# Optimization experiments

Measured on AMD Instinct MI355X. Metric: run time of the kernel, lower is better.

Reference implementation:

```python
import jax, jax.numpy as jnp
import numpy as np
from jax import lax

B, N, CH, CIN, H, W = 4, 256, 128, 1024, 120, 160
SRC = 256      # source rows of the (B, CH, 256, 1) relation feature map
MIN_BOX = 5    # boxes smaller than this (at half res) are skipped


def _conv(x, w, b):
    # 3x3 SAME conv, NCHW / OIHW, matching torch Conv2d(pad=1)
    return lax.conv_general_dilated(x, w, (1, 1), 'SAME',
                                    dimension_numbers=('NCHW', 'OIHW', 'NCHW')) + b[None, :, None, None]


def _boxes(k, xmax, ymax):
    k1, k2, k3, k4 = jax.random.split(k, 4)
    x1 = jax.random.randint(k1, (B, N), 0, xmax - 40)
    y1 = jax.random.randint(k2, (B, N), 0, ymax - 40)
    x2 = jnp.clip(x1 + jax.random.randint(k3, (B, N), 10, 80), 0, xmax)
    y2 = jnp.clip(y1 + jax.random.randint(k4, (B, N), 10, 80), 0, ymax)
    return jnp.stack([x1, y1, x2, y2], -1)


def setup_inputs() -> dict:
    key = jax.random.key(0)
    ks = jax.random.split(key, 24)
    s = 0.05
    rn = lambda k, shp: (s * jax.random.normal(k, shp)).astype(jnp.float32)
    return {
        'range_attention_maps': jax.random.normal(ks[0], (B, CH, H, W), jnp.float32),
        'tuple_features': jax.random.normal(ks[1], (B, CIN, N), jnp.float32),
        # rel_embedding: two 1x1 convs stored as matrices
        'rel_w1': rn(ks[2], (CH, CIN)), 'rel_b1': rn(ks[3], (CH,)),
        'rel_w2': rn(ks[4], (CH, CH)),  'rel_b2': rn(ks[5], (CH,)),
        'dmc_w': rn(ks[6], (4, 2 * CH, CH, 3, 3)), 'dmc_b': rn(ks[7], (4, 2 * CH)),
        # TriGraph image collectors: [0,1] Conv2d(2ch->ch), [2,3] Conv2d(ch->ch)
        'imc_w01': rn(ks[8], (2, CH, 2 * CH, 3, 3)), 'imc_b01': rn(ks[9], (2, CH)),
        'imc_w23': rn(ks[10], (2, CH, CH, 3, 3)),    'imc_b23': rn(ks[11], (2, CH)),
        # TriGraph relation collectors: same layout as image collectors
        'rmc_w01': rn(ks[12], (2, CH, 2 * CH, 3, 3)), 'rmc_b01': rn(ks[13], (2, CH)),
        'rmc_w23': rn(ks[14], (2, CH, CH, 3, 3)),     'rmc_b23': rn(ks[15], (2, CH)),
        # final embedding: Conv2d(2ch->ch,3) -> ReLU -> Conv2d(ch->ch,3)
        'emb_w1': rn(ks[16], (CH, 2 * CH, 3, 3)), 'emb_b1': rn(ks[17], (CH,)),
        'emb_w2': rn(ks[18], (CH, CH, 3, 3)),     'emb_b2': rn(ks[19], (CH,)),
        # bbox: [sx1,sy1,sx2,sy2, ox1,oy1,ox2,oy2] at full res (coords < 2W x 2H)
        'bbox': jnp.concatenate([_boxes(ks[20], 2 * W, 2 * H),
                                 _boxes(ks[21], 2 * W, 2 * H)], -1).astype(jnp.int32),
    }


def _interp_scatter(rel_map, bbox):
    # rel_map: (B, CH, SRC) -- the (SRC,1) relation feature map per image.
    # torch F.interpolate(mode='nearest') of a (SRC,1) map to (h,w): column 0 is
    # replicated across width; output row k reads source row floor(k*SRC/h).
    sub = bbox[..., :4] // 2
    obj = bbox[..., 4:] // 2
    sh, sw = sub[..., 3] - sub[..., 1], sub[..., 2] - sub[..., 0]
    oh, ow = obj[..., 3] - obj[..., 1], obj[..., 2] - obj[..., 0]
    # the torch loop `continue`s unless BOTH sub and obj boxes are big enough
    valid = (sh >= MIN_BOX) & (sw >= MIN_BOX) & (oh >= MIN_BOX) & (ow >= MIN_BOX)

    ys = jnp.arange(H)
    xs = jnp.arange(W)
    bi = jnp.arange(B)[:, None, None]

    def contrib(box, h):
        x1, y1, x2, y2 = box[..., 0], box[..., 1], box[..., 2], box[..., 3]
        ym = (ys >= y1[..., None]) & (ys < y2[..., None]) & valid[..., None]   # (B,N,H)
        xm = ((xs >= x1[..., None]) & (xs < x2[..., None])).astype(rel_map.dtype)  # (B,N,W)
        idx = jnp.clip((ys - y1[..., None]) * SRC // jnp.maximum(h, 1)[..., None], 0, SRC - 1)
        rows = rel_map[bi, :, idx] * ym[..., None].astype(rel_map.dtype)       # (B,N,H,CH)
        # scatter-add every box's resized patch into the full map
        return jnp.einsum('bjyc,bjx->bcyx', rows, xm)

    return contrib(sub, sh) + contrib(obj, oh)  # (B, CH, H, W)


def reference(range_attention_maps, tuple_features,
              rel_w1, rel_b1, rel_w2, rel_b2,
              dmc_w, dmc_b, imc_w01, imc_b01, imc_w23, imc_b23,
              rmc_w01, rmc_b01, rmc_w23, rmc_b23,
              emb_w1, emb_b1, emb_w2, emb_b2, bbox):
    relu = jax.nn.relu
    # rel_embedding on (B, CIN, N, 1): 1x1 convs == channel matmuls
    hmid = relu(jnp.einsum('oc,bcn->bon', rel_w1, tuple_features) + rel_b1[None, :, None])
    rel_map = jnp.einsum('oc,bcn->bon', rel_w2, hmid) + rel_b2[None, :, None]  # (B,CH,SRC)

    rel = _interp_scatter(rel_map, bbox)          # (B,CH,H,W)
    img = range_attention_maps                    # (B,CH,H,W)
    dep = jnp.concatenate([img, rel], axis=1)     # (B,2CH,H,W)

    # TriGraph, max_iters = 2; all messages computed from pre-update state
    for i in range(2):
        dm = (_conv(img, dmc_w[i], dmc_b[i]) + _conv(rel, dmc_w[2 + i], dmc_b[2 + i])) * 0.5
        im = (_conv(dep, imc_w01[i], imc_b01[i]) + _conv(rel, imc_w23[i], imc_b23[i])) * 0.5
        rm = (_conv(dep, rmc_w01[i], rmc_b01[i]) + _conv(img, rmc_w23[i], rmc_b23[i])) * 0.5
        dep = relu(dep + dm)
        img = relu(img + im)
        rel = relu(rel + rm)

    out = _conv(relu(_conv(dep, emb_w1, emb_b1)), emb_w2, emb_b2)  # (B,CH,H,W)
    return out
```

## Files before the change

kernel.cpp:

```cpp
#include <hip/hip_runtime.h>

#define BB 4
#define NTUP 256
#define CHN 128
#define CINN 1024
#define HH 120
#define WW 160
#define HWSZ (HH*WW)
#define SRCN 256
#define CT 512

typedef __attribute__((ext_vector_type(8))) _Float16 f16x8;
typedef __attribute__((ext_vector_type(4))) float f32x4;

__device__ __forceinline__ unsigned short f2h(float f) {
  _Float16 h = (_Float16)f;
  return __builtin_bit_cast(unsigned short, h);
}
__device__ __forceinline__ float h2f(unsigned short u) {
  _Float16 h = __builtin_bit_cast(_Float16, u);
  return (float)h;
}

__global__ __launch_bounds__(256) void k_hmid(const float* __restrict__ tf,
    const float* __restrict__ w1, const float* __restrict__ b1,
    float* __restrict__ hmid) {
  int bc = blockIdx.x;
  int b = bc >> 7, c = bc & 127;
  int n = threadIdx.x;
  const float* wrow = w1 + (size_t)c * CINN;
  const float* xcol = tf + (size_t)b * CINN * NTUP + n;
  float acc = 0.f;
#pragma unroll 4
  for (int k = 0; k < CINN; ++k)
    acc += wrow[k] * xcol[(size_t)k * NTUP];
  acc += b1[c];
  hmid[(size_t)bc * NTUP + n] = fmaxf(acc, 0.f);
}

__global__ __launch_bounds__(256) void k_w2t(const float* __restrict__ w2,
                                             float* __restrict__ w2t) {
  int i = blockIdx.x * 256 + threadIdx.x;
  if (i >= CHN * CHN) return;
  int o = i >> 7, c = i & 127;
  w2t[c * CHN + o] = w2[i];
}

__global__ __launch_bounds__(128) void k_relmap(const float* __restrict__ hmid,
    const float* __restrict__ w2t, const float* __restrict__ b2,
    float* __restrict__ rmT) {
  int n = blockIdx.x, b = blockIdx.y, o = threadIdx.x;
  const float* hc = hmid + (size_t)b * CHN * NTUP + n;
  float acc = 0.f;
#pragma unroll 4
  for (int c = 0; c < CHN; ++c)
    acc += hc[(size_t)c * NTUP] * w2t[c * CHN + o];
  rmT[((size_t)b * SRCN + n) * CHN + o] = acc + b2[o];
}

__global__ __launch_bounds__(256) void k_img_init(const float* __restrict__ img,
                                                  unsigned short* __restrict__ S) {
  int xt = blockIdx.x;
  int y  = blockIdx.y;
  int b  = blockIdx.z;
  __shared__ float t[128 * 33];
  int x0 = xt * 32;
  for (int i = threadIdx.x; i < 128 * 32; i += 256) {
    int c = i >> 5, x = i & 31;
    t[c * 33 + x] = img[(((size_t)b * CHN + c) * HH + y) * WW + x0 + x];
  }
  __syncthreads();
  for (int j = threadIdx.x; j < 32 * 128; j += 256) {
    int x = j >> 7, c = j & 127;
    unsigned short v = f2h(t[c * 33 + x]);
    size_t base = ((size_t)b * HWSZ + (size_t)y * WW + x0 + x) * CT;
    S[base + c] = v;
    S[base + 256 + c] = v;
  }
}

__global__ __launch_bounds__(256) void k_scatter(const float* __restrict__ rmT,
    const int* __restrict__ bbox, unsigned short* __restrict__ S) {
  int y  = blockIdx.x;
  int b  = blockIdx.y;
  int x0 = blockIdx.z * 80;
  __shared__ float row[80 * 129];
  int t = threadIdx.x;
  int c = t & 127, xo = t >> 7;
  for (int i = t; i < 80 * 128; i += 256) { int x = i >> 7, cc = i & 127; row[x * 129 + cc] = 0.f; }
  __syncthreads();
  const int* bb = bbox + (size_t)b * NTUP * 8;
  for (int j = 0; j < NTUP; ++j) {
    const int* bp = bb + j * 8;
    int sx1 = bp[0] >> 1, sy1 = bp[1] >> 1, sx2 = bp[2] >> 1, sy2 = bp[3] >> 1;
    int ox1 = bp[4] >> 1, oy1 = bp[5] >> 1, ox2 = bp[6] >> 1, oy2 = bp[7] >> 1;
    int sh = sy2 - sy1, sw = sx2 - sx1, oh = oy2 - oy1, ow = ox2 - ox1;
    if (!((sh >= 5) && (sw >= 5) && (oh >= 5) && (ow >= 5))) continue;
    if (y >= sy1 && y < sy2) {
      int a = max(sx1, x0), e = min(sx2, x0 + 80);
      if (a < e) {
        int idx = min((y - sy1) * SRCN / sh, SRCN - 1);
        float col = rmT[((size_t)b * SRCN + idx) * CHN + c];
        int start = a + ((xo - a) & 1);
        for (int x = start; x < e; x += 2) row[(x - x0) * 129 + c] += col;
      }
    }
    if (y >= oy1 && y < oy2) {
      int a = max(ox1, x0), e = min(ox2, x0 + 80);
      if (a < e) {
        int idx = min((y - oy1) * SRCN / oh, SRCN - 1);
        float col = rmT[((size_t)b * SRCN + idx) * CHN + c];
        int start = a + ((xo - a) & 1);
        for (int x = start; x < e; x += 2) row[(x - x0) * 129 + c] += col;
      }
    }
  }
  __syncthreads();
  for (int j2 = t; j2 < 80 * 128; j2 += 256) {
    int x = j2 >> 7, c2 = j2 & 127;
    unsigned short v = f2h(row[x * 129 + c2]);
    size_t base = ((size_t)b * HWSZ + (size_t)y * WW + x0 + x) * CT;
    S[base + 128 + c2] = v;
    S[base + 384 + c2] = v;
  }
}

__global__ void k_pack(const float* __restrict__ wA, int ICa,
                       const float* __restrict__ wB, int ICb,
                       int OC, unsigned short* __restrict__ dst) {
  int ICP = ICa + ICb;
  int total = 9 * OC * ICP;
  int i = blockIdx.x * 256 + threadIdx.x;
  if (i >= total) return;
  int tap = i / (OC * ICP); int r = i % (OC * ICP);
  int oc = r / ICP; int icp = r % ICP;
  int dy = tap / 3, dx = tap % 3;
  float v;
  if (icp < ICa) v = wA[((size_t)(oc * ICa + icp) * 3 + dy) * 3 + dx];
  else           v = wB[((size_t)(oc * ICb + (icp - ICa)) * 3 + dy) * 3 + dx];
  dst[i] = f2h(v);
}

struct ConvGroup {
  const unsigned short* w;
  const float* biasA;
  const float* biasB;
  const unsigned short* res;
  int ICP, OCg, oc_wbase;
  int c0a, na, c0b;
  int res_c0, out_c0;
  float scale;
  int relu;
};
struct ConvCommon {
  const unsigned short* in; int Ct_in;
  unsigned short* outb; int Ct_out;
  float* outf;
};
struct ConvParams { ConvCommon c; ConvGroup g[4]; };

__global__ __launch_bounds__(512) void k_conv(ConvParams P) {
  const ConvGroup G = P.g[blockIdx.z];
  const int b  = blockIdx.y;
  const int y0 = blockIdx.x * 2;
  const int t = threadIdx.x;
  const int wave = t >> 6, lane = t & 63;
  const int wm = wave & 1, wn = wave >> 1;
  const int r = wn >> 1;
  const int xbase = (wn & 1) * 80;
  const int ln = lane & 15, kg = lane >> 4;

  __shared__ unsigned short lds[4 * 162 * 32];

  f32x4 acc[4][5];
#pragma unroll
  for (int m = 0; m < 4; ++m)
#pragma unroll
    for (int n = 0; n < 5; ++n) acc[m][n] = (f32x4)(0.f);

  const int nch = G.ICP >> 5;
  for (int k = 0; k < nch; ++k) {
    const int icp0 = k << 5;
    const int cg = (icp0 < G.na) ? (G.c0a + icp0) : (G.c0b + icp0 - G.na);
    __syncthreads();
    if (t < 32) {
      int icg = t & 3, hx = (t >> 2) & 1, rw = t >> 3;
      uint4 z = {0u, 0u, 0u, 0u};
      *(uint4*)&lds[((rw * 162) + (hx ? 161 : 0)) * 32 + icg * 8] = z;
    }
#pragma unroll
    for (int s = 0; s < 5; ++s) {
      int id = t + (s << 9);
      int icg = id & 3;
      int xx = (id >> 2) % 160;
      int rw = (id >> 2) / 160;
      int ry = y0 - 1 + rw;
      uint4 v = {0u, 0u, 0u, 0u};
      if (ry >= 0 && ry < HH)
        v = *(const uint4*)(P.c.in + ((size_t)b * HWSZ + (size_t)ry * WW + xx) * P.c.Ct_in + cg + icg * 8);
      *(uint4*)&lds[((rw * 162) + xx + 1) * 32 + icg * 8] = v;
    }
    __syncthreads();
#pragma unroll
    for (int dy = 0; dy < 3; ++dy) {
      const int lrow = (r + dy) * 162;
#pragma unroll
      for (int dx = 0; dx < 3; ++dx) {
        const int tap = dy * 3 + dx;
        const unsigned short* wp = G.w +
            ((size_t)(tap * G.OCg + G.oc_wbase + wm * 64 + ln)) * G.ICP + icp0 + kg * 8;
        f16x8 A[4];
#pragma unroll
        for (int m = 0; m < 4; ++m)
          A[m] = *(const f16x8*)(wp + (size_t)m * 16 * G.ICP);
#pragma unroll
        for (int nf = 0; nf < 5; ++nf) {
          const f16x8 Bv = *(const f16x8*)(&lds[(lrow + xbase + nf * 16 + dx + ln) * 32 + kg * 8]);
#pragma unroll
          for (int m = 0; m < 4; ++m)
            acc[m][nf] = __builtin_amdgcn_mfma_f32_16x16x32_f16(A[m], Bv, acc[m][nf], 0, 0, 0);
        }
      }
    }
  }

  const int yy = y0 + r;
#pragma unroll
  for (int m = 0; m < 4; ++m) {
    const int ocl = wm * 64 + m * 16 + (kg << 2);
    const int ocw = G.oc_wbase + ocl;
    float bias[4];
#pragma unroll
    for (int q = 0; q < 4; ++q)
      bias[q] = G.biasA[ocw + q] + (G.biasB ? G.biasB[ocw + q] : 0.f);
#pragma unroll
    for (int nf = 0; nf < 5; ++nf) {
      const int x = xbase + nf * 16 + ln;
      const size_t pix = (size_t)b * HWSZ + (size_t)yy * WW + x;
      float v[4];
#pragma unroll
      for (int q = 0; q < 4; ++q)
        v[q] = (acc[m][nf][q] + bias[q]) * G.scale;
      if (G.res) {
        const unsigned short* rp = G.res + pix * P.c.Ct_in + G.res_c0 + ocw;
        uint2 rv = *(const uint2*)rp;
        v[0] += h2f((unsigned short)(rv.x & 0xffffu));
        v[1] += h2f((unsigned short)(rv.x >> 16));
        v[2] += h2f((unsigned short)(rv.y & 0xffffu));
        v[3] += h2f((unsigned short)(rv.y >> 16));
      }
      if (G.relu) {
#pragma unroll
        for (int q = 0; q < 4; ++q) v[q] = fmaxf(v[q], 0.f);
      }
      if (P.c.outf) {
#pragma unroll
        for (int q = 0; q < 4; ++q)
          P.c.outf[(((size_t)b * CHN + ocw + q) * HH + yy) * WW + x] = v[q];
      } else {
        uint2 pk;
        pk.x = (unsigned)f2h(v[0]) | ((unsigned)f2h(v[1]) << 16);
        pk.y = (unsigned)f2h(v[2]) | ((unsigned)f2h(v[3]) << 16);
        *(uint2*)(P.c.outb + pix * P.c.Ct_out + G.out_c0 + ocw) = pk;
      }
    }
  }
}

extern "C" void kernel_launch(void* const* d_in, const int* in_sizes, int n_in,
                              void* d_out, int out_size, void* d_ws, size_t ws_size,
                              hipStream_t stream) {
  const float* ram     = (const float*)d_in[0];
  const float* tf      = (const float*)d_in[1];
  const float* w1      = (const float*)d_in[2];
  const float* b1      = (const float*)d_in[3];
  const float* w2      = (const float*)d_in[4];
  const float* b2      = (const float*)d_in[5];
  const float* dmc_w   = (const float*)d_in[6];
  const float* dmc_b   = (const float*)d_in[7];
  const float* imc_w01 = (const float*)d_in[8];
  const float* imc_b01 = (const float*)d_in[9];
  const float* imc_w23 = (const float*)d_in[10];
  const float* imc_b23 = (const float*)d_in[11];
  const float* rmc_w01 = (const float*)d_in[12];
  const float* rmc_b01 = (const float*)d_in[13];
  const float* rmc_w23 = (const float*)d_in[14];
  const float* rmc_b23 = (const float*)d_in[15];
  const float* emb_w1  = (const float*)d_in[16];
  const float* emb_b1  = (const float*)d_in[17];
  const float* emb_w2  = (const float*)d_in[18];
  const float* emb_b2  = (const float*)d_in[19];
  const int*   bbox    = (const int*)d_in[20];
  float* out = (float*)d_out;

  char* ws = (char*)d_ws;
  size_t off = 0;
  auto alloc = [&](size_t bytes) -> void* {
    void* p = ws + off;
    off += (bytes + 255) & ~(size_t)255;
    return p;
  };
  unsigned short* SA = (unsigned short*)alloc((size_t)BB * HWSZ * CT * 2);
  unsigned short* SB = (unsigned short*)alloc((size_t)BB * HWSZ * CT * 2);
  unsigned short* T  = (unsigned short*)alloc((size_t)BB * HWSZ * 128 * 2);
  float* hmid = (float*)alloc((size_t)BB * CHN * NTUP * 4);
  float* rmT  = (float*)alloc((size_t)BB * SRCN * CHN * 4);
  float* w2t  = (float*)alloc((size_t)CHN * CHN * 4);
  unsigned short* pw_dm[2], *pw_im[2], *pw_rm[2];
  for (int i = 0; i < 2; ++i) pw_dm[i] = (unsigned short*)alloc((size_t)9 * 256 * 256 * 2);
  for (int i = 0; i < 2; ++i) pw_im[i] = (unsigned short*)alloc((size_t)9 * 128 * 384 * 2);
  for (int i = 0; i < 2; ++i) pw_rm[i] = (unsigned short*)alloc((size_t)9 * 128 * 384 * 2);
  unsigned short* pw_e1 = (unsigned short*)alloc((size_t)9 * 128 * 256 * 2);
  unsigned short* pw_e2 = (unsigned short*)alloc((size_t)9 * 128 * 128 * 2);
  if (off > ws_size) return;

  k_hmid<<<BB * CHN, 256, 0, stream>>>(tf, w1, b1, hmid);
  k_w2t<<<(CHN * CHN + 255) / 256, 256, 0, stream>>>(w2, w2t);
  k_relmap<<<dim3(NTUP, BB), 128, 0, stream>>>(hmid, w2t, b2, rmT);
  k_img_init<<<dim3(5, HH, BB), 256, 0, stream>>>(ram, SA);
  k_scatter<<<dim3(HH, BB, 2), 256, 0, stream>>>(rmT, bbox, SA);

  auto pk = [&](const float* wA, int ICa, const float* wB, int ICb, int OC,
                unsigned short* dst) {
    int total = 9 * OC * (ICa + ICb);
    k_pack<<<(total + 255) / 256, 256, 0, stream>>>(wA, ICa, wB, ICb, OC, dst);
  };
  for (int i = 0; i < 2; ++i) {
    pk(dmc_w + (size_t)i * 256 * 128 * 9, 128, dmc_w + (size_t)(2 + i) * 256 * 128 * 9, 128, 256, pw_dm[i]);
    pk(imc_w01 + (size_t)i * 128 * 256 * 9, 256, imc_w23 + (size_t)i * 128 * 128 * 9, 128, 128, pw_im[i]);
    pk(rmc_w01 + (size_t)i * 128 * 256 * 9, 256, rmc_w23 + (size_t)i * 128 * 128 * 9, 128, 128, pw_rm[i]);
  }
  pk(emb_w1, 256, nullptr, 0, 128, pw_e1);
  pk(emb_w2, 128, nullptr, 0, 128, pw_e2);

  for (int i = 0; i < 2; ++i) {
    const unsigned short* Sin = (i == 0) ? SA : SB;
    unsigned short* Sout      = (i == 0) ? SB : SA;
    ConvParams cp;
    cp.c.in = Sin; cp.c.Ct_in = CT; cp.c.outb = Sout; cp.c.Ct_out = CT; cp.c.outf = nullptr;
    for (int h = 0; h < 2; ++h) {
      ConvGroup& g = cp.g[h];
      g.w = pw_dm[i]; g.biasA = dmc_b + (size_t)i * 256; g.biasB = dmc_b + (size_t)(2 + i) * 256;
      g.res = Sin; g.ICP = 256; g.OCg = 256; g.oc_wbase = h * 128;
      g.c0a = 256; g.na = 128; g.c0b = 384;
      g.res_c0 = 0; g.out_c0 = 0; g.scale = 0.5f; g.relu = 1;
    }
    {
      ConvGroup& g = cp.g[2];
      g.w = pw_im[i]; g.biasA = imc_b01 + (size_t)i * 128; g.biasB = imc_b23 + (size_t)i * 128;
      g.res = Sin; g.ICP = 384; g.OCg = 128; g.oc_wbase = 0;
      g.c0a = 0; g.na = 256; g.c0b = 384;
      g.res_c0 = 256; g.out_c0 = 256; g.scale = 0.5f; g.relu = 1;
    }
    {
      ConvGroup& g = cp.g[3];
      g.w = pw_rm[i]; g.biasA = rmc_b01 + (size_t)i * 128; g.biasB = rmc_b23 + (size_t)i * 128;
      g.res = Sin; g.ICP = 384; g.OCg = 128; g.oc_wbase = 0;
      g.c0a = 0; g.na = 256; g.c0b = 256;
      g.res_c0 = 384; g.out_c0 = 384; g.scale = 0.5f; g.relu = 1;
    }
    k_conv<<<dim3(HH / 2, BB, 4), 512, 0, stream>>>(cp);
  }

  {
    ConvParams cp;
    cp.c.in = SA; cp.c.Ct_in = CT; cp.c.outb = T; cp.c.Ct_out = 128; cp.c.outf = nullptr;
    ConvGroup& g = cp.g[0];
    g.w = pw_e1; g.biasA = emb_b1; g.biasB = nullptr; g.res = nullptr;
    g.ICP = 256; g.OCg = 128; g.oc_wbase = 0;
    g.c0a = 0; g.na = 256; g.c0b = 0;
    g.res_c0 = -1; g.out_c0 = 0; g.scale = 1.f; g.relu = 1;
    k_conv<<<dim3(HH / 2, BB, 1), 512, 0, stream>>>(cp);
  }
  {
    ConvParams cp;
    cp.c.in = T; cp.c.Ct_in = 128; cp.c.outb = nullptr; cp.c.Ct_out = 0; cp.c.outf = out;
    ConvGroup& g = cp.g[0];
    g.w = pw_e2; g.biasA = emb_b2; g.biasB = nullptr; g.res = nullptr;
    g.ICP = 128; g.OCg = 128; g.oc_wbase = 0;
    g.c0a = 0; g.na = 128; g.c0b = 0;
    g.res_c0 = -1; g.out_c0 = 0; g.scale = 1.f; g.relu = 0;
    k_conv<<<dim3(HH / 2, BB, 1), 512, 0, stream>>>(cp);
  }
}
```

Baseline: 1.494 ms.

## Use channel-blocked activation layout and fragment-packed weights in conv kernel

```diff
diff --git a/kernel.cpp b/kernel.cpp
--- a/kernel.cpp
+++ b/kernel.cpp
@@ -8,7 +8,8 @@
 #define WW 160
 #define HWSZ (HH*WW)
 #define SRCN 256
-#define CT 512
+#define ROWH (WW*32)
+#define CBS  (HH*ROWH)
 
 typedef __attribute__((ext_vector_type(8))) _Float16 f16x8;
 typedef __attribute__((ext_vector_type(4))) float f32x4;
@@ -73,9 +74,9 @@
   for (int j = threadIdx.x; j < 32 * 128; j += 256) {
     int x = j >> 7, c = j & 127;
     unsigned short v = f2h(t[c * 33 + x]);
-    size_t base = ((size_t)b * HWSZ + (size_t)y * WW + x0 + x) * CT;
-    S[base + c] = v;
-    S[base + 256 + c] = v;
+    size_t base = (((size_t)b * 16 + (c >> 5)) * HH + y) * ROWH + (size_t)(x0 + x) * 32 + (c & 31);
+    S[base] = v;
+    S[base + (size_t)8 * CBS] = v;
   }
 }
 
@@ -119,9 +120,9 @@
   for (int j2 = t; j2 < 80 * 128; j2 += 256) {
     int x = j2 >> 7, c2 = j2 & 127;
     unsigned short v = f2h(row[x * 129 + c2]);
-    size_t base = ((size_t)b * HWSZ + (size_t)y * WW + x0 + x) * CT;
-    S[base + 128 + c2] = v;
-    S[base + 384 + c2] = v;
+    size_t base = (((size_t)b * 16 + 4 + (c2 >> 5)) * HH + y) * ROWH + (size_t)(x0 + x) * 32 + (c2 & 31);
+    S[base] = v;
+    S[base + (size_t)8 * CBS] = v;
   }
 }
 
@@ -129,11 +130,19 @@
                        const float* __restrict__ wB, int ICb,
                        int OC, unsigned short* __restrict__ dst) {
   int ICP = ICa + ICb;
+  int ICB = ICP >> 5, OCB = OC >> 4;
   int total = 9 * OC * ICP;
   int i = blockIdx.x * 256 + threadIdx.x;
   if (i >= total) return;
-  int tap = i / (OC * ICP); int r = i % (OC * ICP);
-  int oc = r / ICP; int icp = r % ICP;
+  int j = i & 7;
+  int l = (i >> 3) & 63;
+  int fi = i >> 9;
+  int icb = fi % ICB;
+  int t2 = fi / ICB;
+  int ocb = t2 % OCB;
+  int tap = t2 / OCB;
+  int oc = ocb * 16 + (l & 15);
+  int icp = icb * 32 + (l >> 4) * 8 + j;
   int dy = tap / 3, dx = tap % 3;
   float v;
   if (icp < ICa) v = wA[((size_t)(oc * ICa + icp) * 3 + dy) * 3 + dx];
@@ -153,16 +162,20 @@
   int relu;
 };
 struct ConvCommon {
-  const unsigned short* in; int Ct_in;
-  unsigned short* outb; int Ct_out;
+  const unsigned short* in; int nbin;
+  unsigned short* outb; int nbout;
   float* outf;
+  int nz;
 };
 struct ConvParams { ConvCommon c; ConvGroup g[4]; };
 
 __global__ __launch_bounds__(512) void k_conv(ConvParams P) {
-  const ConvGroup G = P.g[blockIdx.z];
-  const int b  = blockIdx.y;
-  const int y0 = blockIdx.x * 2;
+  const int gid = blockIdx.x;
+  const int z = gid % P.c.nz;
+  const int rest = gid / P.c.nz;
+  const int b = rest & 3;
+  const int y0 = (rest >> 2) * 2;
+  const ConvGroup G = P.g[z];
   const int t = threadIdx.x;
   const int wave = t >> 6, lane = t & 63;
   const int wm = wave & 1, wn = wave >> 1;
@@ -179,26 +192,29 @@
     for (int n = 0; n < 5; ++n) acc[m][n] = (f32x4)(0.f);
 
   const int nch = G.ICP >> 5;
+  const int ICB = G.ICP >> 5;
+  const int OCB = G.OCg >> 4;
   for (int k = 0; k < nch; ++k) {
     const int icp0 = k << 5;
     const int cg = (icp0 < G.na) ? (G.c0a + icp0) : (G.c0b + icp0 - G.na);
+    const int cblk = cg >> 5;
+    const unsigned short* cbase = P.c.in + (((size_t)b * P.c.nbin + cblk) * HH) * ROWH;
     __syncthreads();
     if (t < 32) {
       int icg = t & 3, hx = (t >> 2) & 1, rw = t >> 3;
-      uint4 z = {0u, 0u, 0u, 0u};
-      *(uint4*)&lds[((rw * 162) + (hx ? 161 : 0)) * 32 + icg * 8] = z;
+      uint4 z4 = {0u, 0u, 0u, 0u};
+      *(uint4*)&lds[((rw * 162) + (hx ? 161 : 0)) * 32 + icg * 8] = z4;
     }
 #pragma unroll
     for (int s = 0; s < 5; ++s) {
-      int id = t + (s << 9);
-      int icg = id & 3;
-      int xx = (id >> 2) % 160;
-      int rw = (id >> 2) / 160;
+      int u = t + (s << 9);
+      int rw = u / 640;
+      int rem = u - rw * 640;
       int ry = y0 - 1 + rw;
       uint4 v = {0u, 0u, 0u, 0u};
       if (ry >= 0 && ry < HH)
-        v = *(const uint4*)(P.c.in + ((size_t)b * HWSZ + (size_t)ry * WW + xx) * P.c.Ct_in + cg + icg * 8);
-      *(uint4*)&lds[((rw * 162) + xx + 1) * 32 + icg * 8] = v;
+        v = *(const uint4*)(cbase + (size_t)ry * ROWH + rem * 8);
+      *(uint4*)&lds[rw * 5184 + 32 + rem * 8] = v;
     }
     __syncthreads();
 #pragma unroll
@@ -207,12 +223,12 @@
 #pragma unroll
       for (int dx = 0; dx < 3; ++dx) {
         const int tap = dy * 3 + dx;
-        const unsigned short* wp = G.w +
-            ((size_t)(tap * G.OCg + G.oc_wbase + wm * 64 + ln)) * G.ICP + icp0 + kg * 8;
+        const size_t frag0 = ((size_t)(tap * OCB + (G.oc_wbase >> 4) + wm * 4) * ICB + k) << 9;
+        const unsigned short* wp = G.w + frag0 + lane * 8;
         f16x8 A[4];
 #pragma unroll
         for (int m = 0; m < 4; ++m)
-          A[m] = *(const f16x8*)(wp + (size_t)m * 16 * G.ICP);
+          A[m] = *(const f16x8*)(wp + ((size_t)m * ICB << 9));
 #pragma unroll
         for (int nf = 0; nf < 5; ++nf) {
           const f16x8 Bv = *(const f16x8*)(&lds[(lrow + xbase + nf * 16 + dx + ln) * 32 + kg * 8]);
@@ -236,13 +252,14 @@
 #pragma unroll
     for (int nf = 0; nf < 5; ++nf) {
       const int x = xbase + nf * 16 + ln;
-      const size_t pix = (size_t)b * HWSZ + (size_t)yy * WW + x;
       float v[4];
 #pragma unroll
       for (int q = 0; q < 4; ++q)
         v[q] = (acc[m][nf][q] + bias[q]) * G.scale;
       if (G.res) {
-        const unsigned short* rp = G.res + pix * P.c.Ct_in + G.res_c0 + ocw;
+        const int rc = G.res_c0 + ocw;
+        const unsigned short* rp = G.res +
+            (((size_t)b * P.c.nbin + (rc >> 5)) * HH + yy) * ROWH + (size_t)x * 32 + (rc & 31);
         uint2 rv = *(const uint2*)rp;
         v[0] += h2f((unsigned short)(rv.x & 0xffffu));
         v[1] += h2f((unsigned short)(rv.x >> 16));
@@ -258,10 +275,12 @@
         for (int q = 0; q < 4; ++q)
           P.c.outf[(((size_t)b * CHN + ocw + q) * HH + yy) * WW + x] = v[q];
       } else {
+        const int ow = G.out_c0 + ocw;
         uint2 pk;
         pk.x = (unsigned)f2h(v[0]) | ((unsigned)f2h(v[1]) << 16);
         pk.y = (unsigned)f2h(v[2]) | ((unsigned)f2h(v[3]) << 16);
-        *(uint2*)(P.c.outb + pix * P.c.Ct_out + G.out_c0 + ocw) = pk;
+        *(uint2*)(P.c.outb +
+            (((size_t)b * P.c.nbout + (ow >> 5)) * HH + yy) * ROWH + (size_t)x * 32 + (ow & 31)) = pk;
       }
     }
   }
@@ -300,9 +319,9 @@
     off += (bytes + 255) & ~(size_t)255;
     return p;
   };
-  unsigned short* SA = (unsigned short*)alloc((size_t)BB * HWSZ * CT * 2);
-  unsigned short* SB = (unsigned short*)alloc((size_t)BB * HWSZ * CT * 2);
-  unsigned short* T  = (unsigned short*)alloc((size_t)BB * HWSZ * 128 * 2);
+  unsigned short* SA = (unsigned short*)alloc((size_t)BB * 16 * CBS * 2);
+  unsigned short* SB = (unsigned short*)alloc((size_t)BB * 16 * CBS * 2);
+  unsigned short* T  = (unsigned short*)alloc((size_t)BB * 4 * CBS * 2);
   float* hmid = (float*)alloc((size_t)BB * CHN * NTUP * 4);
   float* rmT  = (float*)alloc((size_t)BB * SRCN * CHN * 4);
   float* w2t  = (float*)alloc((size_t)CHN * CHN * 4);
@@ -337,7 +356,8 @@
     const unsigned short* Sin = (i == 0) ? SA : SB;
     unsigned short* Sout      = (i == 0) ? SB : SA;
     ConvParams cp;
-    cp.c.in = Sin; cp.c.Ct_in = CT; cp.c.outb = Sout; cp.c.Ct_out = CT; cp.c.outf = nullptr;
+    cp.c.in = Sin; cp.c.nbin = 16; cp.c.outb = Sout; cp.c.nbout = 16;
+    cp.c.outf = nullptr; cp.c.nz = 4;
     for (int h = 0; h < 2; ++h) {
       ConvGroup& g = cp.g[h];
       g.w = pw_dm[i]; g.biasA = dmc_b + (size_t)i * 256; g.biasB = dmc_b + (size_t)(2 + i) * 256;
@@ -359,27 +379,29 @@
       g.c0a = 0; g.na = 256; g.c0b = 256;
       g.res_c0 = 384; g.out_c0 = 384; g.scale = 0.5f; g.relu = 1;
     }
-    k_conv<<<dim3(HH / 2, BB, 4), 512, 0, stream>>>(cp);
+    k_conv<<<(HH / 2) * BB * 4, 512, 0, stream>>>(cp);
   }
 
   {
     ConvParams cp;
-    cp.c.in = SA; cp.c.Ct_in = CT; cp.c.outb = T; cp.c.Ct_out = 128; cp.c.outf = nullptr;
+    cp.c.in = SA; cp.c.nbin = 16; cp.c.outb = T; cp.c.nbout = 4;
+    cp.c.outf = nullptr; cp.c.nz = 1;
     ConvGroup& g = cp.g[0];
     g.w = pw_e1; g.biasA = emb_b1; g.biasB = nullptr; g.res = nullptr;
     g.ICP = 256; g.OCg = 128; g.oc_wbase = 0;
     g.c0a = 0; g.na = 256; g.c0b = 0;
     g.res_c0 = -1; g.out_c0 = 0; g.scale = 1.f; g.relu = 1;
-    k_conv<<<dim3(HH / 2, BB, 1), 512, 0, stream>>>(cp);
+    k_conv<<<(HH / 2) * BB, 512, 0, stream>>>(cp);
   }
   {
     ConvParams cp;
-    cp.c.in = T; cp.c.Ct_in = 128; cp.c.outb = nullptr; cp.c.Ct_out = 0; cp.c.outf = out;
+    cp.c.in = T; cp.c.nbin = 4; cp.c.outb = nullptr; cp.c.nbout = 0;
+    cp.c.outf = out; cp.c.nz = 1;
     ConvGroup& g = cp.g[0];
     g.w = pw_e2; g.biasA = emb_b2; g.biasB = nullptr; g.res = nullptr;
     g.ICP = 128; g.OCg = 128; g.oc_wbase = 0;
     g.c0a = 0; g.na = 128; g.c0b = 0;
     g.res_c0 = -1; g.out_c0 = 0; g.scale = 1.f; g.relu = 0;
-    k_conv<<<dim3(HH / 2, BB, 1), 512, 0, stream>>>(cp);
-  }
-}
+    k_conv<<<(HH / 2) * BB, 512, 0, stream>>>(cp);
+  }
+}
```

Measured after the change: 1.195 ms. 20.0% less time.
